# Optimization experiments

Measured on AMD Instinct MI355X. Metric: run time of the kernel, lower is better.

The kernel has to match this reference:

```python
import jax, jax.numpy as jnp
import numpy as np


def log_g(x):
    # log of g(x) = x+0.5 if x>=0 else sigmoid(x), computed stably
    return jnp.where(x >= 0, jnp.log(jax.nn.relu(x) + 0.5), -jax.nn.softplus(-x))


def setup_inputs() -> dict:
    key = jax.random.key(0)
    ks = jax.random.split(key, 6)
    B, S, D, H = 8, 4096, 1024, 1024
    scale = 1.0 / np.sqrt(D)
    return {
        "x": jax.random.normal(ks[0], (B, S, D), dtype=jnp.float32),
        "h0": jax.random.normal(ks[1], (B, 1, H), dtype=jnp.float32),
        "Wz": jax.random.normal(ks[2], (H, D), dtype=jnp.float32) * scale,
        "bz": jax.random.normal(ks[3], (H,), dtype=jnp.float32) * scale,
        "Wh": jax.random.normal(ks[4], (H, D), dtype=jnp.float32) * scale,
        "bh": jax.random.normal(ks[5], (H,), dtype=jnp.float32) * scale,
    }


def reference(x, h0, Wz, bz, Wh, bh):
    # x: (B,S,D), h0: (B,1,H)
    k = jnp.einsum("bsd,hd->bsh", x, Wz) + bz            # linear_z
    log_z = -jax.nn.softplus(-k)                          # log sigmoid(k)
    log_coeffs = -jax.nn.softplus(k)                      # log (1 - sigmoid(k))
    log_h0 = log_g(h0)                                    # (B,1,H)
    log_tilde_h = log_g(jnp.einsum("bsd,hd->bsh", x, Wh) + bh)
    log_values = jnp.concatenate([log_h0, log_z + log_tilde_h], axis=1)  # (B,S+1,H)
    a_star = jnp.pad(jnp.cumsum(log_coeffs, axis=1), ((0, 0), (1, 0), (0, 0)))  # (B,S+1,H)
    log_h0_plus_b_star = jax.lax.cumlogsumexp(log_values - a_star, axis=1)
    h = jnp.exp(a_star[:, 1:] + log_h0_plus_b_star[:, 1:])  # (B,S,H)
    return h
```

## Files before the change

### kernel.cpp

```cpp
#include <hip/hip_runtime.h>
#include <cstdint>
#include <cstddef>

#define B_  8
#define S_  4096
#define D_  1024
#define H_  1024
#define M_  (B_*S_)
#define NC_ 64
#define L_  (S_/NC_)

typedef __bf16 bf16x8 __attribute__((ext_vector_type(8)));
typedef float  f32x4  __attribute__((ext_vector_type(4)));
typedef uint16_t u16x8 __attribute__((ext_vector_type(8)));

__device__ __forceinline__ uint16_t f2bf(float f) {
  union { float f; uint32_t u; } v; v.f = f;
  uint32_t u = v.u;
  u += 0x7FFFu + ((u >> 16) & 1u);
  return (uint16_t)(u >> 16);
}
__device__ __forceinline__ float gfun(float x) {
  return x >= 0.0f ? x + 0.5f
                   : __builtin_amdgcn_rcpf(1.0f + __expf(-x));
}
__device__ __forceinline__ void unpack_cv(uint32_t u, float& c, float& v) {
  union { uint32_t u; _Float16 h[2]; } p; p.u = u;
  c = (float)p.h[0]; v = (float)p.h[1];
}

#define X8_  (M_ * D_ / 8)
#define W8_  (H_ * D_ / 8)
#define TOT8_ (X8_ + 2 * W8_)
__global__ __launch_bounds__(256) void cvt_all_kernel(
    const float* __restrict__ x, const float* __restrict__ Wz,
    const float* __restrict__ Wh, uint16_t* __restrict__ xb,
    uint16_t* __restrict__ Wzb, uint16_t* __restrict__ Whb) {
  int stride = gridDim.x * 256;
  for (int u = blockIdx.x * 256 + threadIdx.x; u < TOT8_; u += stride) {
    const float* src; uint16_t* dst;
    if (u < X8_)            { src = x  + (size_t)u * 8;          dst = xb  + (size_t)u * 8; }
    else if (u < X8_ + W8_) { size_t v = u - X8_;        src = Wz + v * 8; dst = Wzb + v * 8; }
    else                    { size_t v = u - X8_ - W8_;  src = Wh + v * 8; dst = Whb + v * 8; }
    float4 a = ((const float4*)src)[0], b = ((const float4*)src)[1];
    u16x8 o;
    o[0] = f2bf(a.x); o[1] = f2bf(a.y); o[2] = f2bf(a.z); o[3] = f2bf(a.w);
    o[4] = f2bf(b.x); o[5] = f2bf(b.y); o[6] = f2bf(b.z); o[7] = f2bf(b.w);
    *(u16x8*)dst = o;
  }
}

#define BM 128
#define BNH 128
#define BK 64
__global__ __launch_bounds__(256, 2)
void fused_gemm_kernel(const uint16_t* __restrict__ A,
                       const uint16_t* __restrict__ Wz,
                       const uint16_t* __restrict__ Wh,
                       const float* __restrict__ bz,
                       const float* __restrict__ bh,
                       uint32_t* __restrict__ cv) {
  __shared__ __attribute__((aligned(16))) uint16_t As[BM * BK];
  __shared__ __attribute__((aligned(16))) uint16_t Bzs[BNH * BK];
  __shared__ __attribute__((aligned(16))) uint16_t Bhs[BNH * BK];
  const int tid  = threadIdx.x;
  const int lane = tid & 63;
  const int wave = tid >> 6;
  const int mTile = blockIdx.y * BM;
  const int nTile = blockIdx.x * BNH;
  const int wm0 = (wave >> 1) * 64;
  const int wn0 = (wave & 1) * 64;
  const int q  = lane >> 4;
  const int mn = lane & 15;

  const uint16_t* aPtr[4];
  const uint16_t* zPtr[4];
  const uint16_t* hPtr[4];
  #pragma unroll
  for (int i = 0; i < 4; i++) {
    int u = i * 256 + tid;
    int r = u >> 3;
    int c = (u & 7) ^ (r & 7);
    aPtr[i] = A  + (size_t)(mTile + r) * D_ + c * 8;
    zPtr[i] = Wz + (size_t)(nTile + r) * D_ + c * 8;
    hPtr[i] = Wh + (size_t)(nTile + r) * D_ + c * 8;
  }
  const int ldsDst = (wave * 64 + lane) * 8;

  f32x4 accK[4][4] = {};
  f32x4 accP[4][4] = {};

  for (int kt = 0; kt < D_; kt += BK) {
    __syncthreads();
    #pragma unroll
    for (int i = 0; i < 4; i++)
      __builtin_amdgcn_global_load_lds(
          (const __attribute__((address_space(1))) void*)(aPtr[i] + kt),
          (__attribute__((address_space(3))) void*)&As[i * 2048 + ldsDst], 16, 0, 0);
    #pragma unroll
    for (int i = 0; i < 4; i++)
      __builtin_amdgcn_global_load_lds(
          (const __attribute__((address_space(1))) void*)(zPtr[i] + kt),
          (__attribute__((address_space(3))) void*)&Bzs[i * 2048 + ldsDst], 16, 0, 0);
    #pragma unroll
    for (int i = 0; i < 4; i++)
      __builtin_amdgcn_global_load_lds(
          (const __attribute__((address_space(1))) void*)(hPtr[i] + kt),
          (__attribute__((address_space(3))) void*)&Bhs[i * 2048 + ldsDst], 16, 0, 0);
    __syncthreads();

    #pragma unroll
    for (int s = 0; s < 2; s++) {
      bf16x8 av[4], bzv[4], bhv[4];
      const int cu = s * 4 + q;
      #pragma unroll
      for (int tm = 0; tm < 4; tm++) {
        int r = wm0 + tm * 16 + mn;
        av[tm] = *(const bf16x8*)&As[(r * 8 + (cu ^ (r & 7))) * 8];
      }
      #pragma unroll
      for (int tn = 0; tn < 4; tn++) {
        int r = wn0 + tn * 16 + mn;
        int unit = r * 8 + (cu ^ (r & 7));
        bzv[tn] = *(const bf16x8*)&Bzs[unit * 8];
        bhv[tn] = *(const bf16x8*)&Bhs[unit * 8];
      }
      #pragma unroll
      for (int tm = 0; tm < 4; tm++)
        #pragma unroll
        for (int tn = 0; tn < 4; tn++) {
          accK[tm][tn] = __builtin_amdgcn_mfma_f32_16x16x32_bf16(
              av[tm], bzv[tn], accK[tm][tn], 0, 0, 0);
          accP[tm][tn] = __builtin_amdgcn_mfma_f32_16x16x32_bf16(
              av[tm], bhv[tn], accP[tm][tn], 0, 0, 0);
        }
    }
  }

  #pragma unroll
  for (int tn = 0; tn < 4; tn++) {
    int col = nTile + wn0 + tn * 16 + mn;
    float bzc = bz[col], bhc = bh[col];
    #pragma unroll
    for (int tm = 0; tm < 4; tm++) {
      int row0 = mTile + wm0 + tm * 16 + q * 4;
      #pragma unroll
      for (int i = 0; i < 4; i++) {
        float kv = accK[tm][tn][i] + bzc;
        float pv = accP[tm][tn][i] + bhc;
        float c = __builtin_amdgcn_rcpf(1.0f + __expf(kv));
        float z = 1.0f - c;
        float v = z * gfun(pv);
        union { _Float16 h[2]; uint32_t u; } pk;
        pk.h[0] = (_Float16)c; pk.h[1] = (_Float16)v;
        cv[(size_t)(row0 + i) * H_ + col] = pk.u;
      }
    }
  }
}

__global__ __launch_bounds__(256) void scan_chunk_kernel(
    const uint32_t* __restrict__ cv, float4* __restrict__ Cc,
    float4* __restrict__ Vc) {
  const int tid = threadIdx.x;
  const int nc = blockIdx.x, b = blockIdx.y;
  const uint4* cv4 = (const uint4*)cv;
  size_t base = (size_t)(b * S_ + nc * L_) * (H_ / 4) + tid;
  float C[4] = {1.f, 1.f, 1.f, 1.f};
  float V[4] = {0.f, 0.f, 0.f, 0.f};
  #pragma unroll 4
  for (int t = 0; t < L_; t++) {
    uint4 w = cv4[base + (size_t)t * (H_ / 4)];
    float c, v;
    unpack_cv(w.x, c, v); C[0] *= c; V[0] = c * V[0] + v;
    unpack_cv(w.y, c, v); C[1] *= c; V[1] = c * V[1] + v;
    unpack_cv(w.z, c, v); C[2] *= c; V[2] = c * V[2] + v;
    unpack_cv(w.w, c, v); C[3] *= c; V[3] = c * V[3] + v;
  }
  size_t o = (size_t)(b * NC_ + nc) * (H_ / 4) + tid;
  Cc[o] = (float4){C[0], C[1], C[2], C[3]};
  Vc[o] = (float4){V[0], V[1], V[2], V[3]};
}

__global__ __launch_bounds__(256) void scan_apply_kernel(
    const uint32_t* __restrict__ cv, const float4* __restrict__ Cc,
    const float4* __restrict__ Vc, const float* __restrict__ h0,
    float4* __restrict__ out) {
  const int tid = threadIdx.x;
  const int nc = blockIdx.x, b = blockIdx.y;
  const uint4* cv4 = (const uint4*)cv;

  float Hr[4];
  #pragma unroll
  for (int j = 0; j < 4; j++) Hr[j] = gfun(h0[(size_t)b * H_ + tid * 4 + j]);
  #pragma unroll 4
  for (int j = 0; j < nc; j++) {
    size_t idx = (size_t)(b * NC_ + j) * (H_ / 4) + tid;
    float4 Cq = Cc[idx], Vq = Vc[idx];
    Hr[0] = Cq.x * Hr[0] + Vq.x;
    Hr[1] = Cq.y * Hr[1] + Vq.y;
    Hr[2] = Cq.z * Hr[2] + Vq.z;
    Hr[3] = Cq.w * Hr[3] + Vq.w;
  }

  size_t base = (size_t)(b * S_ + nc * L_) * (H_ / 4) + tid;
  #pragma unroll 4
  for (int t = 0; t < L_; t++) {
    size_t idx = base + (size_t)t * (H_ / 4);
    uint4 w = cv4[idx];
    float c, v;
    unpack_cv(w.x, c, v); Hr[0] = c * Hr[0] + v;
    unpack_cv(w.y, c, v); Hr[1] = c * Hr[1] + v;
    unpack_cv(w.z, c, v); Hr[2] = c * Hr[2] + v;
    unpack_cv(w.w, c, v); Hr[3] = c * Hr[3] + v;
    out[idx] = (float4){Hr[0], Hr[1], Hr[2], Hr[3]};
  }
}

extern "C" void kernel_launch(void* const* d_in, const int* in_sizes, int n_in,
                              void* d_out, int out_size, void* d_ws, size_t ws_size,
                              hipStream_t stream) {
  const float* x  = (const float*)d_in[0];
  const float* h0 = (const float*)d_in[1];
  const float* Wz = (const float*)d_in[2];
  const float* bz = (const float*)d_in[3];
  const float* Wh = (const float*)d_in[4];
  const float* bh = (const float*)d_in[5];
  float* out = (float*)d_out;

  char* ws = (char*)d_ws;
  uint16_t* xb  = (uint16_t*)ws; ws += (size_t)M_ * D_ * 2;
  uint16_t* Wzb = (uint16_t*)ws; ws += (size_t)H_ * D_ * 2;
  uint16_t* Whb = (uint16_t*)ws; ws += (size_t)H_ * D_ * 2;
  uint32_t* cvb = (uint32_t*)ws; ws += (size_t)M_ * H_ * 4;
  char* alias = (char*)xb;
  float* Cc  = (float*)alias; alias += (size_t)B_ * NC_ * H_ * 4;
  float* Vc  = (float*)alias; alias += (size_t)B_ * NC_ * H_ * 4;

  cvt_all_kernel<<<dim3(2048), 256, 0, stream>>>(x, Wz, Wh, xb, Wzb, Whb);

  fused_gemm_kernel<<<dim3(H_ / BNH, M_ / BM), 256, 0, stream>>>(
      xb, Wzb, Whb, bz, bh, cvb);

  scan_chunk_kernel<<<dim3(NC_, B_), 256, 0, stream>>>(cvb, (float4*)Cc, (float4*)Vc);
  scan_apply_kernel<<<dim3(NC_, B_), 256, 0, stream>>>(
      cvb, (const float4*)Cc, (const float4*)Vc, h0, (float4*)out);
}
```

Before: 444.2 us.

## Interleave Wz/Wh into one weight matrix and use double-buffered 256x256 GEMM tiles

The weight conversion now writes Wz and Wh interleaved in 16-row groups into a single 2048-row matrix, so the GEMM treats both projections as one N=2048 problem. The GEMM kernel moves to 512 threads with 256x256 tiles and double-buffered LDS staged through global_load_lds. It uses explicit vmcnt waits, barriers, setprio and a grouped block-to-tile mapping to overlap loads with MFMA work. The aim is more data reuse per tile and hidden global-load latency, at the cost of larger LDS use and register pressure plus a fragile hand-written wait schedule.

```diff
diff --git a/kernel.cpp b/kernel.cpp
--- a/kernel.cpp
+++ b/kernel.cpp
@@ -7,6 +7,7 @@
 #define D_  1024
 #define H_  1024
 #define M_  (B_*S_)
+#define NT_ 2048
 #define NC_ 64
 #define L_  (S_/NC_)
 
@@ -35,13 +36,25 @@
 __global__ __launch_bounds__(256) void cvt_all_kernel(
     const float* __restrict__ x, const float* __restrict__ Wz,
     const float* __restrict__ Wh, uint16_t* __restrict__ xb,
-    uint16_t* __restrict__ Wzb, uint16_t* __restrict__ Whb) {
+    uint16_t* __restrict__ Wc) {
   int stride = gridDim.x * 256;
   for (int u = blockIdx.x * 256 + threadIdx.x; u < TOT8_; u += stride) {
     const float* src; uint16_t* dst;
-    if (u < X8_)            { src = x  + (size_t)u * 8;          dst = xb  + (size_t)u * 8; }
-    else if (u < X8_ + W8_) { size_t v = u - X8_;        src = Wz + v * 8; dst = Wzb + v * 8; }
-    else                    { size_t v = u - X8_ - W8_;  src = Wh + v * 8; dst = Whb + v * 8; }
+    if (u < X8_) {
+      src = x + (size_t)u * 8; dst = xb + (size_t)u * 8;
+    } else if (u < X8_ + W8_) {
+      int v = u - X8_;
+      int r = v >> 7, c = v & 127;
+      int row = ((r >> 4) << 5) | (r & 15);
+      src = Wz + (size_t)v * 8;
+      dst = Wc + (size_t)row * D_ + c * 8;
+    } else {
+      int v = u - X8_ - W8_;
+      int r = v >> 7, c = v & 127;
+      int row = ((r >> 4) << 5) | 16 | (r & 15);
+      src = Wh + (size_t)v * 8;
+      dst = Wc + (size_t)row * D_ + c * 8;
+    }
     float4 a = ((const float4*)src)[0], b = ((const float4*)src)[1];
     u16x8 o;
     o[0] = f2bf(a.x); o[1] = f2bf(a.y); o[2] = f2bf(a.z); o[3] = f2bf(a.w);
@@ -50,110 +63,172 @@
   }
 }
 
-#define BM 128
-#define BNH 128
 #define BK 64
-__global__ __launch_bounds__(256, 2)
+__global__ __launch_bounds__(512, 2)
 void fused_gemm_kernel(const uint16_t* __restrict__ A,
-                       const uint16_t* __restrict__ Wz,
-                       const uint16_t* __restrict__ Wh,
+                       const uint16_t* __restrict__ Wc,
                        const float* __restrict__ bz,
                        const float* __restrict__ bh,
                        uint32_t* __restrict__ cv) {
-  __shared__ __attribute__((aligned(16))) uint16_t As[BM * BK];
-  __shared__ __attribute__((aligned(16))) uint16_t Bzs[BNH * BK];
-  __shared__ __attribute__((aligned(16))) uint16_t Bhs[BNH * BK];
+  __shared__ __attribute__((aligned(16))) uint16_t sA[2][256 * BK];
+  __shared__ __attribute__((aligned(16))) uint16_t sB[2][256 * BK];
+
   const int tid  = threadIdx.x;
   const int lane = tid & 63;
   const int wave = tid >> 6;
-  const int mTile = blockIdx.y * BM;
-  const int nTile = blockIdx.x * BNH;
-  const int wm0 = (wave >> 1) * 64;
-  const int wn0 = (wave & 1) * 64;
+  const int wm = wave >> 2;
+  const int wn = wave & 3;
   const int q  = lane >> 4;
   const int mn = lane & 15;
 
-  const uint16_t* aPtr[4];
-  const uint16_t* zPtr[4];
-  const uint16_t* hPtr[4];
+  const int bid  = blockIdx.x;
+  const int tile = (bid & 7) * 128 + (bid >> 3);
+  const int mTile = (tile >> 3) * 256;
+  const int nTile = (tile & 7) * 256;
+
+  const int rl = tid >> 3;
+  const int cu = tid & 7;
+  const int sw = cu ^ (rl & 7);
+  const uint16_t* aSrc[4];
+  const uint16_t* bSrc[4];
   #pragma unroll
-  for (int i = 0; i < 4; i++) {
-    int u = i * 256 + tid;
-    int r = u >> 3;
-    int c = (u & 7) ^ (r & 7);
-    aPtr[i] = A  + (size_t)(mTile + r) * D_ + c * 8;
-    zPtr[i] = Wz + (size_t)(nTile + r) * D_ + c * 8;
-    hPtr[i] = Wh + (size_t)(nTile + r) * D_ + c * 8;
-  }
-  const int ldsDst = (wave * 64 + lane) * 8;
-
-  f32x4 accK[4][4] = {};
-  f32x4 accP[4][4] = {};
-
-  for (int kt = 0; kt < D_; kt += BK) {
-    __syncthreads();
+  for (int L = 0; L < 4; L++) {
+    aSrc[L] = A  + (size_t)(mTile + L * 64 + rl) * D_ + sw * 8;
+    bSrc[L] = Wc + (size_t)(nTile + L * 64 + rl) * D_ + sw * 8;
+  }
+  const int ldsSlot = tid * 8;
+
+  const int swr = mn & 7;
+  const int aBase = (wm * 128 + mn) * 64;
+  const int bBase = (wn * 64  + mn) * 64;
+  int koff[2];
+  #pragma unroll
+  for (int kk = 0; kk < 2; kk++) koff[kk] = ((kk * 4 + q) ^ swr) * 8;
+
+#define STAGE_A(buf, kt, L)                                                    \
+  __builtin_amdgcn_global_load_lds(                                            \
+      (const __attribute__((address_space(1))) void*)(aSrc[L] + (kt) * BK),    \
+      (__attribute__((address_space(3))) void*)&sA[buf][(L) * 4096 + ldsSlot], \
+      16, 0, 0)
+#define STAGE_B(buf, kt, L)                                                    \
+  __builtin_amdgcn_global_load_lds(                                            \
+      (const __attribute__((address_space(1))) void*)(bSrc[L] + (kt) * BK),    \
+      (__attribute__((address_space(3))) void*)&sB[buf][(L) * 4096 + ldsSlot], \
+      16, 0, 0)
+
+  f32x4 acc[8][4] = {};
+
+  STAGE_A(0, 0, 0); STAGE_A(0, 0, 2);
+  STAGE_B(0, 0, 0); STAGE_B(0, 0, 1); STAGE_B(0, 0, 2); STAGE_B(0, 0, 3);
+  STAGE_A(0, 0, 1); STAGE_A(0, 0, 3);
+  STAGE_A(1, 1, 0); STAGE_A(1, 1, 2);
+  STAGE_B(1, 1, 0); STAGE_B(1, 1, 1); STAGE_B(1, 1, 2); STAGE_B(1, 1, 3);
+  STAGE_A(1, 1, 1); STAGE_A(1, 1, 3);
+  asm volatile("s_waitcnt vmcnt(8)" ::: "memory");
+  __builtin_amdgcn_s_barrier();
+
+  #pragma unroll 2
+  for (int t = 0; t < D_ / BK - 1; ++t) {
+    const int curb = t & 1, nxtb = curb ^ 1;
+    const uint16_t* sAc = sA[curb];
+    const uint16_t* sBc = sB[curb];
+    const bool doStage = (t >= 1);
+    const int kn = t + 1;
+
+    bf16x8 bv[4][2];
+
     #pragma unroll
-    for (int i = 0; i < 4; i++)
-      __builtin_amdgcn_global_load_lds(
-          (const __attribute__((address_space(1))) void*)(aPtr[i] + kt),
-          (__attribute__((address_space(3))) void*)&As[i * 2048 + ldsDst], 16, 0, 0);
+    for (int p = 0; p < 4; ++p) {
+      if (p == 0) {
+        #pragma unroll
+        for (int tn = 0; tn < 4; tn++)
+          #pragma unroll
+          for (int kk = 0; kk < 2; kk++)
+            bv[tn][kk] = *(const bf16x8*)&sBc[bBase + tn * 1024 + koff[kk]];
+      }
+      bf16x8 av[2][2];
+      #pragma unroll
+      for (int mi = 0; mi < 2; mi++)
+        #pragma unroll
+        for (int kk = 0; kk < 2; kk++)
+          av[mi][kk] =
+              *(const bf16x8*)&sAc[aBase + (2 * p + mi) * 1024 + koff[kk]];
+
+      if (doStage) {
+        if (p == 0) { STAGE_A(nxtb, kn, 0); STAGE_A(nxtb, kn, 2); }
+        if (p == 1) { STAGE_B(nxtb, kn, 0); STAGE_B(nxtb, kn, 1); }
+        if (p == 2) { STAGE_B(nxtb, kn, 2); STAGE_B(nxtb, kn, 3); }
+        if (p == 3) { STAGE_A(nxtb, kn, 1); STAGE_A(nxtb, kn, 3); }
+      }
+
+      __builtin_amdgcn_s_barrier();
+      asm volatile("s_waitcnt lgkmcnt(0)" ::: "memory");
+      __builtin_amdgcn_sched_barrier(0);
+      __builtin_amdgcn_s_setprio(1);
+      #pragma unroll
+      for (int mi = 0; mi < 2; mi++)
+        #pragma unroll
+        for (int tn = 0; tn < 4; tn++)
+          #pragma unroll
+          for (int kk = 0; kk < 2; kk++)
+            acc[2 * p + mi][tn] = __builtin_amdgcn_mfma_f32_16x16x32_bf16(
+                av[mi][kk], bv[tn][kk], acc[2 * p + mi][tn], 0, 0, 0);
+      __builtin_amdgcn_s_setprio(0);
+      __builtin_amdgcn_sched_barrier(0);
+      if (p == 1) asm volatile("s_waitcnt vmcnt(4)" ::: "memory");
+      if (p == 3) asm volatile("s_waitcnt vmcnt(2)" ::: "memory");
+      __builtin_amdgcn_s_barrier();
+    }
+  }
+#undef STAGE_A
+#undef STAGE_B
+
+  asm volatile("s_waitcnt vmcnt(0)" ::: "memory");
+  __builtin_amdgcn_s_barrier();
+  __builtin_amdgcn_sched_barrier(0);
+  {
+    const uint16_t* sAc = sA[1];
+    const uint16_t* sBc = sB[1];
+    bf16x8 bv[4][2];
     #pragma unroll
-    for (int i = 0; i < 4; i++)
-      __builtin_amdgcn_global_load_lds(
-          (const __attribute__((address_space(1))) void*)(zPtr[i] + kt),
-          (__attribute__((address_space(3))) void*)&Bzs[i * 2048 + ldsDst], 16, 0, 0);
+    for (int tn = 0; tn < 4; tn++)
+      #pragma unroll
+      for (int kk = 0; kk < 2; kk++)
+        bv[tn][kk] = *(const bf16x8*)&sBc[bBase + tn * 1024 + koff[kk]];
+    __builtin_amdgcn_s_setprio(1);
     #pragma unroll
-    for (int i = 0; i < 4; i++)
-      __builtin_amdgcn_global_load_lds(
-          (const __attribute__((address_space(1))) void*)(hPtr[i] + kt),
-          (__attribute__((address_space(3))) void*)&Bhs[i * 2048 + ldsDst], 16, 0, 0);
-    __syncthreads();
-
+    for (int m = 0; m < 8; m++) {
+      bf16x8 av[2];
+      #pragma unroll
+      for (int kk = 0; kk < 2; kk++)
+        av[kk] = *(const bf16x8*)&sAc[aBase + m * 1024 + koff[kk]];
+      #pragma unroll
+      for (int tn = 0; tn < 4; tn++)
+        #pragma unroll
+        for (int kk = 0; kk < 2; kk++)
+          acc[m][tn] = __builtin_amdgcn_mfma_f32_16x16x32_bf16(
+              av[kk], bv[tn][kk], acc[m][tn], 0, 0, 0);
+    }
+    __builtin_amdgcn_s_setprio(0);
+  }
+
+  #pragma unroll
+  for (int tp = 0; tp < 2; ++tp) {
+    const int ncol = nTile + wn * 64 + tp * 32;
+    const int h = ((ncol >> 5) << 4) + mn;
+    const float bzc = bz[h], bhc = bh[h];
     #pragma unroll
-    for (int s = 0; s < 2; s++) {
-      bf16x8 av[4], bzv[4], bhv[4];
-      const int cu = s * 4 + q;
-      #pragma unroll
-      for (int tm = 0; tm < 4; tm++) {
-        int r = wm0 + tm * 16 + mn;
-        av[tm] = *(const bf16x8*)&As[(r * 8 + (cu ^ (r & 7))) * 8];
-      }
-      #pragma unroll
-      for (int tn = 0; tn < 4; tn++) {
-        int r = wn0 + tn * 16 + mn;
-        int unit = r * 8 + (cu ^ (r & 7));
-        bzv[tn] = *(const bf16x8*)&Bzs[unit * 8];
-        bhv[tn] = *(const bf16x8*)&Bhs[unit * 8];
-      }
-      #pragma unroll
-      for (int tm = 0; tm < 4; tm++)
-        #pragma unroll
-        for (int tn = 0; tn < 4; tn++) {
-          accK[tm][tn] = __builtin_amdgcn_mfma_f32_16x16x32_bf16(
-              av[tm], bzv[tn], accK[tm][tn], 0, 0, 0);
-          accP[tm][tn] = __builtin_amdgcn_mfma_f32_16x16x32_bf16(
-              av[tm], bhv[tn], accP[tm][tn], 0, 0, 0);
-        }
-    }
-  }
-
-  #pragma unroll
-  for (int tn = 0; tn < 4; tn++) {
-    int col = nTile + wn0 + tn * 16 + mn;
-    float bzc = bz[col], bhc = bh[col];
-    #pragma unroll
-    for (int tm = 0; tm < 4; tm++) {
-      int row0 = mTile + wm0 + tm * 16 + q * 4;
-      #pragma unroll
-      for (int i = 0; i < 4; i++) {
-        float kv = accK[tm][tn][i] + bzc;
-        float pv = accP[tm][tn][i] + bhc;
+    for (int m = 0; m < 8; ++m) {
+      const int row0 = mTile + wm * 128 + m * 16 + q * 4;
+      #pragma unroll
+      for (int i = 0; i < 4; ++i) {
+        float kv = acc[m][2 * tp][i] + bzc;
+        float pv = acc[m][2 * tp + 1][i] + bhc;
         float c = __builtin_amdgcn_rcpf(1.0f + __expf(kv));
-        float z = 1.0f - c;
-        float v = z * gfun(pv);
-        union { _Float16 h[2]; uint32_t u; } pk;
-        pk.h[0] = (_Float16)c; pk.h[1] = (_Float16)v;
-        cv[(size_t)(row0 + i) * H_ + col] = pk.u;
+        float v = (1.0f - c) * gfun(pv);
+        union { _Float16 h2[2]; uint32_t u; } pk;
+        pk.h2[0] = (_Float16)c; pk.h2[1] = (_Float16)v;
+        cv[(size_t)(row0 + i) * H_ + h] = pk.u;
       }
     }
   }
@@ -230,17 +305,16 @@
 
   char* ws = (char*)d_ws;
   uint16_t* xb  = (uint16_t*)ws; ws += (size_t)M_ * D_ * 2;
-  uint16_t* Wzb = (uint16_t*)ws; ws += (size_t)H_ * D_ * 2;
-  uint16_t* Whb = (uint16_t*)ws; ws += (size_t)H_ * D_ * 2;
+  uint16_t* Wcb = (uint16_t*)ws; ws += (size_t)NT_ * D_ * 2;
   uint32_t* cvb = (uint32_t*)ws; ws += (size_t)M_ * H_ * 4;
   char* alias = (char*)xb;
   float* Cc  = (float*)alias; alias += (size_t)B_ * NC_ * H_ * 4;
   float* Vc  = (float*)alias; alias += (size_t)B_ * NC_ * H_ * 4;
 
-  cvt_all_kernel<<<dim3(2048), 256, 0, stream>>>(x, Wz, Wh, xb, Wzb, Whb);
-
-  fused_gemm_kernel<<<dim3(H_ / BNH, M_ / BM), 256, 0, stream>>>(
-      xb, Wzb, Whb, bz, bh, cvb);
+  cvt_all_kernel<<<dim3(2048), 256, 0, stream>>>(x, Wz, Wh, xb, Wcb);
+
+  fused_gemm_kernel<<<dim3((NT_ / 256) * (M_ / 256)), 512, 0, stream>>>(
+      xb, Wcb, bz, bh, cvb);
 
   scan_chunk_kernel<<<dim3(NC_, B_), 256, 0, stream>>>(cvb, (float4*)Cc, (float4*)Vc);
   scan_apply_kernel<<<dim3(NC_, B_), 256, 0, stream>>>(
```

Measured after the change: 435.8 us. About the same (-1.9%).
